# Kernel optimization log

Measured on AMD Instinct MI355X. Metric: run time of the kernel, lower is better.

The kernel has to match this reference:

```python
import jax, jax.numpy as jnp
import numpy as np

B_GRAPHS = 16      # number of graphs in batch
NPG = 8192         # nodes per graph
N = B_GRAPHS * NPG # 131072 total nodes
F_DIM = 64         # node feature dim
K_CLUST = 16       # n_clusters
DEG = 32           # avg degree
E = N * DEG        # 4,194,304 edges


def setup_inputs() -> dict:
    key = jax.random.key(0)
    k1, k2, k3, k4, k5 = jax.random.split(key, 5)
    x = jax.random.normal(k1, (N, F_DIM), jnp.float32)
    W = jax.random.normal(k2, (F_DIM, K_CLUST), jnp.float32) / np.sqrt(F_DIM)
    b = jnp.zeros((K_CLUST,), jnp.float32)
    # edges constrained within each graph -> block-diagonal adjacency (PyG batching)
    g = jnp.repeat(jnp.arange(B_GRAPHS, dtype=jnp.int32), E // B_GRAPHS)
    edge_row = g * NPG + jax.random.randint(k3, (E,), 0, NPG, jnp.int32)
    edge_col = g * NPG + jax.random.randint(k4, (E,), 0, NPG, jnp.int32)
    edge_weight = jax.random.uniform(k5, (E,), jnp.float32)
    return {"x": x, "W": W, "b": b, "edge_weight": edge_weight,
            "edge_row": edge_row, "edge_col": edge_col, "num_graphs": B_GRAPHS}


def _forward(x, W, b, edge_weight, edge_row, edge_col, num_graphs):
    Ntot, Fd = x.shape
    K = W.shape[1]
    Bn = num_graphs
    n = Ntot // Bn  # equal-size graphs (ptr = n * arange(B+1))

    s = x @ W + b                                   # [N,K] cluster logits
    xb = x.reshape(Bn, n, Fd)
    sb = s.reshape(Bn, n, K)
    # out_x = selu(s^T @ x_bd), block b = s_b^T x_b, then hsplit_and_vstack -> [B*K, F]
    out_x = jax.nn.selu(jnp.einsum('bnk,bnf->bkf', sb, xb)).reshape(Bn * K, Fd)

    ss = jax.nn.softmax(s, axis=-1)                 # softmaxed assignments
    ssb = ss.reshape(Bn, n, K)

    # degree d = adj.sum(axis=0)  (column sums over COO edges)
    d = jax.ops.segment_sum(edge_weight, edge_col, num_segments=Ntot)   # [N]
    m2 = d.reshape(Bn, n).sum(1)                    # total degree per graph [B]

    # A @ C via edge scatter: (A C)[row] += w * C[col]
    AC = jax.ops.segment_sum(edge_weight[:, None] * ss[edge_col], edge_row,
                             num_segments=Ntot)     # [N,K]
    # out_adj blocks: C_b^T A_b C_b  -> [B,K,K]
    out_adj = jnp.einsum('bnk,bnl->bkl', ssb, AC.reshape(Bn, n, K))

    # dS_b = C_b^T d_b  (Ca/Cb blocks); normalizer gets m_inv twice in torch code
    dS = jnp.einsum('bn,bnk->bk', d.reshape(Bn, n), ssb)                # [B,K]
    spectral_loss = -jnp.mean(jnp.einsum('bkk->b', out_adj) / m2
                              - (dS ** 2).sum(1) / (m2 ** 2))

    sqrt_K = jnp.sqrt(jnp.float32(K))
    cluster_size = ssb.sum(1)                        # [B,K]
    cluster_loss = jnp.mean(jnp.sqrt((cluster_size ** 2).sum(1)) / n * sqrt_K - 1.0)

    # CC blocks: C_b^T C_b; ortho = mean_b || CC_b/||CC_b||_F - I/sqrt(K) ||_F
    CC = jnp.einsum('bnk,bnl->bkl', ssb, ssb)        # [B,K,K]
    CC_norm = jnp.sqrt((CC ** 2).sum((1, 2)))        # Frobenius norm per block
    eye_div_k = jnp.eye(K, dtype=x.dtype) / sqrt_K
    ortho_loss = jnp.mean(jnp.sqrt(
        ((CC / CC_norm[:, None, None] - eye_div_k) ** 2).sum((1, 2))))

    # mask diagonal and degree-normalize pooled adjacency
    oa = out_adj * (1.0 - jnp.eye(K, dtype=x.dtype))
    dd = jnp.sqrt(oa.sum(2)) + 1e-12                 # row sums per block [B,K]
    out_adj_norm = oa / (dd[:, :, None] * dd[:, None, :])

    return out_x, out_adj_norm, spectral_loss, cluster_loss, ortho_loss


def reference(x, W, b, edge_weight, edge_row, edge_col, num_graphs):
    return _forward(x, W, b, edge_weight, edge_row, edge_col, num_graphs)
```

## Files before the change

kernel.cpp:

```cpp
#include <hip/hip_runtime.h>
#include <math.h>

#define F_DIM 64
#define K_CL 16
#define B_GR 16
#define SROW 72

typedef _Float16 h16;
using f16x4 = __attribute__((ext_vector_type(4))) _Float16;
using f16x8 = __attribute__((ext_vector_type(8))) _Float16;
using f32x4 = __attribute__((ext_vector_type(4))) float;
using fx2   = __attribute__((ext_vector_type(2))) float;
using fp16x2 = __attribute__((ext_vector_type(2))) __fp16;

static __device__ inline unsigned h2u(fp16x2 h) {
    union { fp16x2 h; unsigned u; } x; x.h = h; return x.u;
}

__global__ __launch_bounds__(256) void k_fused(
    const float* __restrict__ x, const float* __restrict__ W, const float* __restrict__ bvec,
    uint4* __restrict__ ssh8, float* __restrict__ outxP, float* __restrict__ CCbP,
    float* __restrict__ oadj)
{
    __shared__ float Wl[F_DIM * K_CL];
    __shared__ float bl[K_CL];
    __shared__ __align__(16) h16 stage[4][(16 + 16 + 64) * SROW];

    int t = threadIdx.x;
    int bid = blockIdx.x;
    if (bid == 0) {
#pragma unroll
        for (int i = 0; i < 16; ++i) oadj[t + i * 256] = 0.f;
    }
    for (int idx = t; idx < F_DIM * K_CL; idx += 256) Wl[idx] = W[idx];
    if (t < K_CL) bl[t] = bvec[t];
    __syncthreads();

    int wid = t >> 6, lane = t & 63;
    h16* Sg = stage[wid];
    h16* Cg = Sg + 16 * SROW;
    h16* Xg = Cg + 16 * SROW;

    size_t i = (size_t)bid * 256 + t;
    float s[16];
#pragma unroll
    for (int k = 0; k < 16; ++k) s[k] = bl[k];

    const float4* xp = reinterpret_cast<const float4*>(x + i * F_DIM);
#pragma unroll
    for (int j = 0; j < 16; ++j) {
        float4 q = xp[j];
        float xf[4] = {q.x, q.y, q.z, q.w};
#pragma unroll
        for (int ff = 0; ff < 4; ++ff) {
            int f = j * 4 + ff;
            float xv = xf[ff];
            Xg[f * SROW + lane] = (h16)xv;
            const float4* wr = reinterpret_cast<const float4*>(&Wl[f * K_CL]);
            float4 w0 = wr[0], w1 = wr[1], w2 = wr[2], w3 = wr[3];
            s[0]  += xv * w0.x; s[1]  += xv * w0.y; s[2]  += xv * w0.z; s[3]  += xv * w0.w;
            s[4]  += xv * w1.x; s[5]  += xv * w1.y; s[6]  += xv * w1.z; s[7]  += xv * w1.w;
            s[8]  += xv * w2.x; s[9]  += xv * w2.y; s[10] += xv * w2.z; s[11] += xv * w2.w;
            s[12] += xv * w3.x; s[13] += xv * w3.y; s[14] += xv * w3.z; s[15] += xv * w3.w;
        }
    }

#pragma unroll
    for (int k = 0; k < 16; ++k) Sg[k * SROW + lane] = (h16)s[k];

    float m = s[0];
#pragma unroll
    for (int k = 1; k < 16; ++k) m = fmaxf(m, s[k]);
    float sum = 0.f;
#pragma unroll
    for (int k = 0; k < 16; ++k) { s[k] = __expf(s[k] - m); sum += s[k]; }
    float inv = 1.0f / sum;
#pragma unroll
    for (int k = 0; k < 16; ++k) s[k] *= inv;

    f16x8 h0, h1;
#pragma unroll
    for (int k = 0; k < 8; ++k) { h0[k] = (h16)s[k]; h1[k] = (h16)s[k + 8]; }
#pragma unroll
    for (int k = 0; k < 8; ++k) {
        Cg[k * SROW + lane] = h0[k];
        Cg[(k + 8) * SROW + lane] = h1[k];
    }

    {
        unsigned d0, d1, d2, d3;
        d0 = __builtin_amdgcn_cvt_pk_fp8_f32(s[0],  s[1],  0,  false);
        d0 = __builtin_amdgcn_cvt_pk_fp8_f32(s[2],  s[3],  d0, true);
        d1 = __builtin_amdgcn_cvt_pk_fp8_f32(s[4],  s[5],  0,  false);
        d1 = __builtin_amdgcn_cvt_pk_fp8_f32(s[6],  s[7],  d1, true);
        d2 = __builtin_amdgcn_cvt_pk_fp8_f32(s[8],  s[9],  0,  false);
        d2 = __builtin_amdgcn_cvt_pk_fp8_f32(s[10], s[11], d2, true);
        d3 = __builtin_amdgcn_cvt_pk_fp8_f32(s[12], s[13], 0,  false);
        d3 = __builtin_amdgcn_cvt_pk_fp8_f32(s[14], s[15], d3, true);
        uint4 pk; pk.x = d0; pk.y = d1; pk.z = d2; pk.w = d3;
        ssh8[i] = pk;
    }

    int q4 = lane >> 4, mm = lane & 15;
    f32x4 accO[4] = {{0.f,0.f,0.f,0.f},{0.f,0.f,0.f,0.f},{0.f,0.f,0.f,0.f},{0.f,0.f,0.f,0.f}};
    f32x4 accC = {0.f, 0.f, 0.f, 0.f};
#pragma unroll
    for (int h = 0; h < 2; ++h) {
        f16x8 aO = *(const f16x8*)&Sg[mm * SROW + h * 32 + q4 * 8];
        f16x8 aC = *(const f16x8*)&Cg[mm * SROW + h * 32 + q4 * 8];
        accC = __builtin_amdgcn_mfma_f32_16x16x32_f16(aC, aC, accC, 0, 0, 0);
#pragma unroll
        for (int ft = 0; ft < 4; ++ft) {
            f16x8 bO = *(const f16x8*)&Xg[(ft * 16 + mm) * SROW + h * 32 + q4 * 8];
            accO[ft] = __builtin_amdgcn_mfma_f32_16x16x32_f16(aO, bO, accO[ft], 0, 0, 0);
        }
    }
    __syncthreads();

    float* redO = (float*)&stage[0][0];
    float* redC = redO + 4096;
#pragma unroll
    for (int ft = 0; ft < 4; ++ft)
#pragma unroll
        for (int rg = 0; rg < 4; ++rg)
            redO[wid * 1024 + (q4 * 4 + rg) * 64 + ft * 16 + mm] = accO[ft][rg];
#pragma unroll
    for (int rg = 0; rg < 4; ++rg)
        redC[wid * 256 + (q4 * 4 + rg) * 16 + mm] = accC[rg];
    __syncthreads();

#pragma unroll
    for (int it = 0; it < 4; ++it) {
        int idx = t + it * 256;
        float v = redO[idx] + redO[1024 + idx] + redO[2048 + idx] + redO[3072 + idx];
        outxP[(size_t)bid * 1024 + idx] = v;
    }
    {
        float v = redC[t] + redC[256 + t] + redC[512 + t] + redC[768 + t];
        CCbP[(size_t)bid * 256 + t] = v;
    }
}

__global__ __launch_bounds__(256) void k_edge(
    const int* __restrict__ erow, const int* __restrict__ ecol, const float* __restrict__ ew,
    const uint4* __restrict__ ssh8, float* __restrict__ oadj,
    int edges_per_block, int edges_per_graph, int nmask)
{
    __shared__ float CCl[256];
    __shared__ __align__(16) h16 stageE[4][2048];
    int t = threadIdx.x;
    CCl[t] = 0.f;
    __syncthreads();

    int bid = blockIdx.x;
    int xcd = bid & 7;
    int slot = bid >> 3;
    int graph = xcd + 8 * (slot & 1);
    int chunk = slot >> 1;

    int wid = t >> 6, lane = t & 63;
    int q4 = lane >> 4, mm = lane & 15;
    h16* Ag = stageE[wid];

    int epw = edges_per_block >> 2;
    int nt  = epw >> 6;
    size_t base = (size_t)graph * edges_per_graph
                + (size_t)chunk * edges_per_block
                + (size_t)wid * epw
                + lane;

    f32x4 acc = {0.f, 0.f, 0.f, 0.f};

    f16x8* Aw = reinterpret_cast<f16x8*>(Ag);
    using lds_h16 = __attribute__((address_space(3))) h16;
    unsigned trA = (unsigned)(uintptr_t)(lds_h16*)Ag + (unsigned)(q4 * 256 + mm * 2);

    auto dec_dw = [](unsigned d, float w, unsigned& o0, unsigned& o1) {
        fx2 p = __builtin_amdgcn_cvt_pk_f32_fp8((int)d, false);
        fx2 q = __builtin_amdgcn_cvt_pk_f32_fp8((int)d, true);
        o0 = h2u(__builtin_amdgcn_cvt_pkrtz(p.x * w, p.y * w));
        o1 = h2u(__builtin_amdgcn_cvt_pkrtz(q.x * w, q.y * w));
    };

    auto compute_tile = [&](uint4 va, uint4 vb, float wv) {
        union { unsigned u[4]; f16x8 v; } alo, ahi, blo, bhi;
        dec_dw(va.x, wv, alo.u[0], alo.u[1]);
        dec_dw(va.y, wv, alo.u[2], alo.u[3]);
        dec_dw(va.z, wv, ahi.u[0], ahi.u[1]);
        dec_dw(va.w, wv, ahi.u[2], ahi.u[3]);
        dec_dw(vb.x, 1.0f, blo.u[0], blo.u[1]);
        dec_dw(vb.y, 1.0f, blo.u[2], blo.u[3]);
        dec_dw(vb.z, 1.0f, bhi.u[0], bhi.u[1]);
        dec_dw(vb.w, 1.0f, bhi.u[2], bhi.u[3]);

        Aw[lane * 2]           = alo.v;
        Aw[lane * 2 + 1]       = ahi.v;
        Aw[128 + lane * 2]     = blo.v;
        Aw[128 + lane * 2 + 1] = bhi.v;

        f16x4 xa0, xa1, xa2, xa3, xb0, xb1, xb2, xb3;
        asm volatile(
            "ds_read_b64_tr_b16 %0, %8\n\t"
            "ds_read_b64_tr_b16 %1, %8 offset:128\n\t"
            "ds_read_b64_tr_b16 %2, %8 offset:2048\n\t"
            "ds_read_b64_tr_b16 %3, %8 offset:2176\n\t"
            "ds_read_b64_tr_b16 %4, %8 offset:1024\n\t"
            "ds_read_b64_tr_b16 %5, %8 offset:1152\n\t"
            "ds_read_b64_tr_b16 %6, %8 offset:3072\n\t"
            "ds_read_b64_tr_b16 %7, %8 offset:3200\n\t"
            "s_waitcnt lgkmcnt(0)"
            : "=&v"(xa0), "=&v"(xa1), "=&v"(xb0), "=&v"(xb1),
              "=&v"(xa2), "=&v"(xa3), "=&v"(xb2), "=&v"(xb3)
            : "v"(trA)
            : "memory");
        __builtin_amdgcn_sched_barrier(0);

        f16x8 afL = __builtin_shufflevector(xa0, xa1, 0, 1, 2, 3, 4, 5, 6, 7);
        f16x8 bfL = __builtin_shufflevector(xb0, xb1, 0, 1, 2, 3, 4, 5, 6, 7);
        f16x8 afH = __builtin_shufflevector(xa2, xa3, 0, 1, 2, 3, 4, 5, 6, 7);
        f16x8 bfH = __builtin_shufflevector(xb2, xb3, 0, 1, 2, 3, 4, 5, 6, 7);
        acc = __builtin_amdgcn_mfma_f32_16x16x32_f16(afL, bfL, acc, 0, 0, 0);
        acc = __builtin_amdgcn_mfma_f32_16x16x32_f16(afH, bfH, acc, 0, 0, 0);
    };

    int rC, cC; float wC;
    rC = erow[base]; cC = ecol[base]; wC = ew[base];
    uint4 ca = ssh8[(size_t)(rC & nmask)];
    uint4 cb = ssh8[(size_t)(cC & nmask)];
    int rN = 0, cN = 0; float wN = 0.f;
    {
        size_t e = base + 64;
        rN = erow[e]; cN = ecol[e]; wN = ew[e];
    }

    for (int tt = 0; tt < nt - 1; ++tt) {
        uint4 na = ssh8[(size_t)(rN & nmask)];
        uint4 nb = ssh8[(size_t)(cN & nmask)];
        int t2 = (tt + 2 < nt) ? (tt + 2) : 0;
        size_t e2 = base + (size_t)t2 * 64;
        int r2 = erow[e2], c2 = ecol[e2];
        float w2 = ew[e2];

        compute_tile(ca, cb, wC);

        ca = na; cb = nb; wC = wN;
        rN = r2; cN = c2; wN = w2;
    }
    compute_tile(ca, cb, wC);

#pragma unroll
    for (int rg = 0; rg < 4; ++rg)
        atomicAdd(&CCl[(q4 * 4 + rg) * 16 + mm], acc[rg]);
    __syncthreads();
    atomicAdd(oadj + graph * 256 + t, CCl[t]);
}

__global__ __launch_bounds__(256) void k_final(
    const float* __restrict__ outxP, const float* __restrict__ oadj,
    const float* __restrict__ CCbP, float* __restrict__ out, int npg)
{
    int t = threadIdx.x;
    int gid = blockIdx.x * 256 + t;
    {
        int g = gid >> 10, idx = gid & 1023;
        const float* p = outxP + (size_t)(g * 32) * 1024 + idx;
        float sv = 0.f;
#pragma unroll
        for (int sub = 0; sub < 32; ++sub) sv += p[(size_t)sub * 1024];
        float r = (sv > 0.f) ? (1.0507009873554805f * sv)
                             : (1.0507009873554805f * 1.6732632423543772f * (__expf(sv) - 1.0f));
        out[gid] = r;
    }

    if (blockIdx.x != 0) return;

    __shared__ float ccred[16 * 256];
    for (int g = 0; g < 16; ++g) {
        const float* p = CCbP + (size_t)(g * 32) * 256 + t;
        float sv = 0.f;
#pragma unroll
        for (int sub = 0; sub < 32; ++sub) sv += p[(size_t)sub * 256];
        ccred[g * 256 + t] = sv;
    }
    __syncthreads();

    int b = t >> 4, k = t & 15;
    const float* oar = oadj + b * 256 + k * 16;
    const float* ccr = &ccred[b * 256 + k * 16];

    float rowsum_off = 0.f, trace_c = 0.f, rowsum_all = 0.f, fro2 = 0.f, colsum = 0.f;
    float csv = 0.f;
#pragma unroll
    for (int l = 0; l < 16; ++l) {
        float v = oar[l];
        rowsum_all += v;
        if (l == k) trace_c = v; else rowsum_off += v;
        float c = ccr[l];
        fro2 += c * c;
        csv += c;
        colsum += oadj[b * 256 + l * 16 + k];
    }
    float dd = sqrtf(rowsum_off) + 1e-12f;
    __shared__ float ddl[B_GR * K_CL];
    ddl[t] = dd;

    float ds2 = colsum * colsum, cs2 = csv * csv;
    float tr = trace_c, m2 = rowsum_all;
#pragma unroll
    for (int msk = 8; msk >= 1; msk >>= 1) {
        tr   += __shfl_xor(tr,   msk, 16);
        ds2  += __shfl_xor(ds2,  msk, 16);
        cs2  += __shfl_xor(cs2,  msk, 16);
        fro2 += __shfl_xor(fro2, msk, 16);
        m2   += __shfl_xor(m2,   msk, 16);
    }
    float invfro = 1.0f / sqrtf(fro2);
    float osum = 0.f;
#pragma unroll
    for (int l = 0; l < 16; ++l) {
        float v = ccr[l] * invfro - ((l == k) ? 0.25f : 0.f);
        osum += v * v;
    }
#pragma unroll
    for (int msk = 8; msk >= 1; msk >>= 1) osum += __shfl_xor(osum, msk, 16);

    __shared__ float sp_s[B_GR], cl_s[B_GR], or_s[B_GR];
    if (k == 0) {
        sp_s[b] = tr / m2 - ds2 / (m2 * m2);
        cl_s[b] = sqrtf(cs2) / (float)npg * 4.0f - 1.0f;
        or_s[b] = sqrtf(osum);
    }
    __syncthreads();
    if (t == 0) {
        float a = 0.f, c = 0.f, o = 0.f;
        for (int i = 0; i < B_GR; ++i) { a += sp_s[i]; c += cl_s[i]; o += or_s[i]; }
        out[20480] = -a / 16.f;
        out[20481] = c / 16.f;
        out[20482] = o / 16.f;
    }

#pragma unroll
    for (int l = 0; l < 16; ++l) {
        float v = (l == k) ? 0.f : oar[l] / (dd * ddl[b * 16 + l]);
        out[16384 + b * 256 + k * 16 + l] = v;
    }
}

extern "C" void kernel_launch(void* const* d_in, const int* in_sizes, int n_in,
                              void* d_out, int out_size, void* d_ws, size_t ws_size,
                              hipStream_t stream)
{
    const float* x    = (const float*)d_in[0];
    const float* W    = (const float*)d_in[1];
    const float* bvec = (const float*)d_in[2];
    const float* ew   = (const float*)d_in[3];
    const int* erow   = (const int*)d_in[4];
    const int* ecol   = (const int*)d_in[5];

    int Ntot = in_sizes[0] / F_DIM;
    size_t E = (size_t)in_sizes[3];
    int npg  = Ntot / B_GR;
    int edges_per_graph = (int)(E / B_GR);
    int nmask = Ntot - 1;
    int nfb   = Ntot / 256;

    const int ADJ_BLOCKS = 2048;
    int edges_per_block = (int)(E / ADJ_BLOCKS);

    char* ws = (char*)d_ws;
    size_t o = 0;
    uint4* ssh8  = (uint4*)(ws + o);    o += (size_t)Ntot * 16;
    float* outxP = (float*)(ws + o);    o += (size_t)nfb * 1024 * 4;
    float* CCbP  = (float*)(ws + o);    o += (size_t)nfb * 256 * 4;
    float* oadj  = (float*)(ws + o);    o += (size_t)B_GR * 256 * 4;

    k_fused<<<nfb, 256, 0, stream>>>(x, W, bvec, ssh8, outxP, CCbP, oadj);
    k_edge<<<ADJ_BLOCKS, 256, 0, stream>>>(erow, ecol, ew, ssh8, oadj,
                                           edges_per_block, edges_per_graph, nmask);
    k_final<<<64, 256, 0, stream>>>(outxP, oadj, CCbP, (float*)d_out, npg);
}
```

Baseline: 175.6 us.

## Move out_x and CC partial reductions into the edge kernel prologue

The cross-block reduction of out_x partials (with SELU) and of the CC partials moves out of k_final and into the first blocks of k_edge, spread across many blocks. k_final shrinks to a single block that only does the small loss and normalisation math. This targets the serial 16-graph CC reduction done by one block in k_final and the separate launch of a 64-block pass. The cost is extra work at the start of some edge blocks, where only 32 threads are active, and an extra workspace buffer.

New measurement: 167.0 us. 4.9% less time.

```diff
diff --git a/kernel.cpp b/kernel.cpp
--- a/kernel.cpp
+++ b/kernel.cpp
@@ -144,6 +144,8 @@
 __global__ __launch_bounds__(256) void k_edge(
     const int* __restrict__ erow, const int* __restrict__ ecol, const float* __restrict__ ew,
     const uint4* __restrict__ ssh8, float* __restrict__ oadj,
+    const float* __restrict__ outxP, const float* __restrict__ CCbP,
+    float* __restrict__ CCb, float* __restrict__ out,
     int edges_per_block, int edges_per_graph, int nmask)
 {
     __shared__ float CCl[256];
@@ -157,6 +159,23 @@
     int slot = bid >> 3;
     int graph = xcd + 8 * (slot & 1);
     int chunk = slot >> 1;
+
+    if (chunk < 32) {
+        if (t < 32) {
+            int idx = chunk * 32 + t;
+            float sv = 0.f;
+            for (int sub = 0; sub < 32; ++sub)
+                sv += outxP[(size_t)(graph * 32 + sub) * 1024 + idx];
+            float r = (sv > 0.f) ? (1.0507009873554805f * sv)
+                                 : (1.0507009873554805f * 1.6732632423543772f * (__expf(sv) - 1.0f));
+            out[graph * 1024 + idx] = r;
+        }
+    } else if (chunk == 32) {
+        float sv = 0.f;
+        for (int sub = 0; sub < 32; ++sub)
+            sv += CCbP[(size_t)(graph * 32 + sub) * 256 + t];
+        CCb[graph * 256 + t] = sv;
+    }
 
     int wid = t >> 6, lane = t & 63;
     int q4 = lane >> 4, mm = lane & 15;
@@ -256,37 +275,13 @@
 }
 
 __global__ __launch_bounds__(256) void k_final(
-    const float* __restrict__ outxP, const float* __restrict__ oadj,
-    const float* __restrict__ CCbP, float* __restrict__ out, int npg)
+    const float* __restrict__ oadj, const float* __restrict__ CCb,
+    float* __restrict__ out, int npg)
 {
     int t = threadIdx.x;
-    int gid = blockIdx.x * 256 + t;
-    {
-        int g = gid >> 10, idx = gid & 1023;
-        const float* p = outxP + (size_t)(g * 32) * 1024 + idx;
-        float sv = 0.f;
-#pragma unroll
-        for (int sub = 0; sub < 32; ++sub) sv += p[(size_t)sub * 1024];
-        float r = (sv > 0.f) ? (1.0507009873554805f * sv)
-                             : (1.0507009873554805f * 1.6732632423543772f * (__expf(sv) - 1.0f));
-        out[gid] = r;
-    }
-
-    if (blockIdx.x != 0) return;
-
-    __shared__ float ccred[16 * 256];
-    for (int g = 0; g < 16; ++g) {
-        const float* p = CCbP + (size_t)(g * 32) * 256 + t;
-        float sv = 0.f;
-#pragma unroll
-        for (int sub = 0; sub < 32; ++sub) sv += p[(size_t)sub * 256];
-        ccred[g * 256 + t] = sv;
-    }
-    __syncthreads();
-
     int b = t >> 4, k = t & 15;
     const float* oar = oadj + b * 256 + k * 16;
-    const float* ccr = &ccred[b * 256 + k * 16];
+    const float* ccr = CCb + b * 256 + k * 16;
 
     float rowsum_off = 0.f, trace_c = 0.f, rowsum_all = 0.f, fro2 = 0.f, colsum = 0.f;
     float csv = 0.f;
@@ -373,9 +368,11 @@
     float* outxP = (float*)(ws + o);    o += (size_t)nfb * 1024 * 4;
     float* CCbP  = (float*)(ws + o);    o += (size_t)nfb * 256 * 4;
     float* oadj  = (float*)(ws + o);    o += (size_t)B_GR * 256 * 4;
+    float* CCb   = (float*)(ws + o);    o += (size_t)B_GR * 256 * 4;
 
     k_fused<<<nfb, 256, 0, stream>>>(x, W, bvec, ssh8, outxP, CCbP, oadj);
     k_edge<<<ADJ_BLOCKS, 256, 0, stream>>>(erow, ecol, ew, ssh8, oadj,
+                                           outxP, CCbP, CCb, (float*)d_out,
                                            edges_per_block, edges_per_graph, nmask);
-    k_final<<<64, 256, 0, stream>>>(outxP, oadj, CCbP, (float*)d_out, npg);
-}
+    k_final<<<1, 256, 0, stream>>>(oadj, CCb, (float*)d_out, npg);
+}
```
